# Kernel tuning notes

Measured on AMD Instinct MI355X. Metric: run time of the kernel, lower is better.

Reference implementation:

```python
import jax, jax.numpy as jnp
import numpy as np

N, BS, DIM, SIZE = 512, 64, 256, 8192

def setup_inputs() -> dict:
    key = jax.random.key(0)
    k1, k2 = jax.random.split(key)
    seq = jax.random.normal(k1, (N, BS, DIM), dtype=jnp.float32)
    # codebook initialized Uniform[-1, 1] as in _reset_parameters
    vocab = jax.random.uniform(k2, (SIZE, DIM), dtype=jnp.float32, minval=-1.0, maxval=1.0)
    return {"seq": seq, "vocab": vocab}

def reference(seq, vocab):
    n, bs, d = seq.shape
    x = seq.reshape(n * bs, d)                                   # [T, D]
    # squared euclidean distances; argmin identical to cdist(p=2).argmin
    x2 = jnp.sum(x * x, axis=-1, keepdims=True)                  # [T, 1]
    v2 = jnp.sum(vocab * vocab, axis=-1)                         # [K]
    d2 = x2 - 2.0 * (x @ vocab.T) + v2                           # [T, K]
    ingredients = jnp.argmin(d2, axis=1)                          # [T]
    out = jnp.take(vocab, ingredients, axis=0).reshape(n, bs, d)  # quantized seq
    return out, ingredients.reshape(n, bs)
```

## Files before the change

### kernel.cpp

```cpp
#include <hip/hip_runtime.h>

#define T_TOTAL 32768
#define D       256
#define K       8192
#define BQ      64
#define KSPLIT  4
#define KSLICE  (K / KSPLIT)
#define NSLICE  (KSPLIT * 4)
#define NCT32   (K / 32)
#define KT_STRIDE (NCT32 * 64 * 8)
#define NQB     (T_TOTAL / BQ)

typedef _Float16 half4f   __attribute__((ext_vector_type(4)));
typedef _Float16 half8f   __attribute__((ext_vector_type(8)));
typedef float    floatx16 __attribute__((ext_vector_type(16)));

#define PARTIAL_F 1048576
#define BHALVES   2097152

__device__ __forceinline__ _Float16 hi16(float x) { return (_Float16)x; }
__device__ __forceinline__ _Float16 lo16(float x, _Float16 h) { return (_Float16)(x - (float)h); }
__device__ __forceinline__ void split4(float4 v, half4f& h, half4f& l) {
    _Float16 hx = hi16(v.x), hy = hi16(v.y), hz = hi16(v.z), hw = hi16(v.w);
    h = (half4f){hx, hy, hz, hw};
    l = (half4f){lo16(v.x, hx), lo16(v.y, hy), lo16(v.z, hz), lo16(v.w, hw)};
}

__global__ void prep_kernel(const float* __restrict__ vocab,
                            _Float16* __restrict__ bhi, _Float16* __restrict__ blo,
                            float* __restrict__ hv2) {
    const int ct = blockIdx.x;
    const int t  = threadIdx.x;
    const int k4 = t & 63;
    const int w  = t >> 6;
    const float4* voc4 = (const float4*)vocab;
    const int kt = k4 >> 2;
    const int q  = k4 & 3;
    const int fl = 32 * (q >> 1);
    const int i0 = (q & 1) * 4;
    float ss[8];
    #pragma unroll
    for (int ci = 0; ci < 8; ++ci) {
        int cc = w * 8 + ci;
        float4 v = voc4[(size_t)(ct * 32 + cc) * (D / 4) + k4];
        half4f hh, ll;
        split4(v, hh, ll);
        size_t off = (((size_t)kt * NCT32 + ct) * 64 + (cc + fl)) * 8 + i0;
        *(half4f*)&bhi[off] = hh;
        *(half4f*)&blo[off] = ll;
        ss[ci] = v.x * v.x + v.y * v.y + v.z * v.z + v.w * v.w;
    }
    #pragma unroll
    for (int ci = 0; ci < 8; ++ci) {
        float s = ss[ci];
        #pragma unroll
        for (int off = 32; off; off >>= 1) s += __shfl_down(s, off, 64);
        if ((t & 63) == 0) hv2[ct * 32 + w * 8 + ci] = 0.5f * s;
    }
}

__launch_bounds__(256, 2)
__global__ void argmin_kernel(const float* __restrict__ seq,
                              const _Float16* __restrict__ bhi,
                              const _Float16* __restrict__ blo,
                              const float* __restrict__ hv2,
                              float2* __restrict__ partial) {
    __shared__ _Float16 AhL[2 * 16 * 64 * 8];
    __shared__ _Float16 AlL[2 * 16 * 64 * 8];

    const int t    = threadIdx.x;
    const int lane = t & 63;
    const int wn   = t >> 6;
    const int bi   = blockIdx.x;
    const int slice = (bi & 7) >> 1;
    const int qb    = (bi >> 3) * 2 + (bi & 1);
    const int q0   = qb * BQ;
    const int k0   = slice * KSLICE;

    const float4* seq4 = (const float4*)seq;

    #pragma unroll
    for (int i = 0; i < 16; ++i) {
        int f   = t + 256 * i;
        int row = f >> 6;
        int d4  = f & 63;
        float4 v = seq4[(size_t)(q0 + row) * (D / 4) + d4];
        half4f h, l;
        split4(v, h, l);
        int kt = d4 >> 2, qq = d4 & 3;
        int off = (((((row >> 5) * 16 + kt) * 64) + ((row & 31) + 32 * (qq >> 1))) * 8
                   + (qq & 1) * 4)
                  ^ (kt << 3);
        *(half4f*)&AhL[off] = h;
        *(half4f*)&AlL[off] = l;
    }
    __syncthreads();

    float best[32];
    int   bidx[32];
    #pragma unroll
    for (int b = 0; b < 32; ++b) { best[b] = 3.4e38f; bidx[b] = 0; }

    const _Float16* bh_l = bhi + (size_t)lane * 8;
    const _Float16* bl_l = blo + (size_t)lane * 8;

    for (int c0i = 0; c0i < KSLICE / 256; ++c0i) {
        const int c0  = k0 + c0i * 256;
        const int ct0 = (c0 >> 5) + wn * 2;
        const size_t cb = (size_t)ct0 * 512;

        floatx16 acc[2][2];
        #pragma unroll
        for (int mi = 0; mi < 2; ++mi)
            #pragma unroll
            for (int nj = 0; nj < 2; ++nj)
                #pragma unroll
                for (int r = 0; r < 16; ++r) acc[mi][nj][r] = 0.0f;

        half8f bh0[2], bl0[2], bh1[2], bl1[2];
        half8f ah0[2], al0[2], ah1[2], al1[2];
        #pragma unroll
        for (int nj = 0; nj < 2; ++nj) {
            bh0[nj] = *(const half8f*)&bh_l[cb + nj * 512];
            bl0[nj] = *(const half8f*)&bl_l[cb + nj * 512];
        }
        #pragma unroll
        for (int mi = 0; mi < 2; ++mi) {
            const int ao = ((mi * 16) * 64 + lane) * 8;
            ah0[mi] = *(const half8f*)&AhL[ao];
            al0[mi] = *(const half8f*)&AlL[ao];
        }

        #pragma unroll 1
        for (int kt2 = 0; kt2 < 8; ++kt2) {
            const int kt = kt2 * 2;
            {
                const size_t kb = (size_t)(kt + 1) * KT_STRIDE + cb;
                #pragma unroll
                for (int nj = 0; nj < 2; ++nj) {
                    bh1[nj] = *(const half8f*)&bh_l[kb + nj * 512];
                    bl1[nj] = *(const half8f*)&bl_l[kb + nj * 512];
                }
                #pragma unroll
                for (int mi = 0; mi < 2; ++mi) {
                    const int ao = (((mi * 16 + kt + 1) * 64 + lane) * 8) ^ ((kt + 1) << 3);
                    ah1[mi] = *(const half8f*)&AhL[ao];
                    al1[mi] = *(const half8f*)&AlL[ao];
                }
            }
            #pragma unroll
            for (int nj = 0; nj < 2; ++nj)
                #pragma unroll
                for (int mi = 0; mi < 2; ++mi)
                    acc[mi][nj] = __builtin_amdgcn_mfma_f32_32x32x16_f16(al0[mi], bh0[nj], acc[mi][nj], 0, 0, 0);
            #pragma unroll
            for (int nj = 0; nj < 2; ++nj)
                #pragma unroll
                for (int mi = 0; mi < 2; ++mi)
                    acc[mi][nj] = __builtin_amdgcn_mfma_f32_32x32x16_f16(ah0[mi], bl0[nj], acc[mi][nj], 0, 0, 0);
            #pragma unroll
            for (int nj = 0; nj < 2; ++nj)
                #pragma unroll
                for (int mi = 0; mi < 2; ++mi)
                    acc[mi][nj] = __builtin_amdgcn_mfma_f32_32x32x16_f16(ah0[mi], bh0[nj], acc[mi][nj], 0, 0, 0);
            if (kt2 < 7) {
                const size_t kb = (size_t)(kt + 2) * KT_STRIDE + cb;
                #pragma unroll
                for (int nj = 0; nj < 2; ++nj) {
                    bh0[nj] = *(const half8f*)&bh_l[kb + nj * 512];
                    bl0[nj] = *(const half8f*)&bl_l[kb + nj * 512];
                }
                #pragma unroll
                for (int mi = 0; mi < 2; ++mi) {
                    const int ao = (((mi * 16 + kt + 2) * 64 + lane) * 8) ^ ((kt + 2) << 3);
                    ah0[mi] = *(const half8f*)&AhL[ao];
                    al0[mi] = *(const half8f*)&AlL[ao];
                }
            }
            #pragma unroll
            for (int nj = 0; nj < 2; ++nj)
                #pragma unroll
                for (int mi = 0; mi < 2; ++mi)
                    acc[mi][nj] = __builtin_amdgcn_mfma_f32_32x32x16_f16(al1[mi], bh1[nj], acc[mi][nj], 0, 0, 0);
            #pragma unroll
            for (int nj = 0; nj < 2; ++nj)
                #pragma unroll
                for (int mi = 0; mi < 2; ++mi)
                    acc[mi][nj] = __builtin_amdgcn_mfma_f32_32x32x16_f16(ah1[mi], bl1[nj], acc[mi][nj], 0, 0, 0);
            #pragma unroll
            for (int nj = 0; nj < 2; ++nj)
                #pragma unroll
                for (int mi = 0; mi < 2; ++mi)
                    acc[mi][nj] = __builtin_amdgcn_mfma_f32_32x32x16_f16(ah1[mi], bh1[nj], acc[mi][nj], 0, 0, 0);
        }

        #pragma unroll
        for (int nj = 0; nj < 2; ++nj) {
            int c = c0 + (wn * 2 + nj) * 32 + (lane & 31);
            float hv = hv2[c];
            #pragma unroll
            for (int mi = 0; mi < 2; ++mi)
                #pragma unroll
                for (int r = 0; r < 16; ++r) {
                    float s = hv - acc[mi][nj][r];
                    int b = mi * 16 + r;
                    if (s < best[b]) { best[b] = s; bidx[b] = c; }
                }
        }
    }

    #pragma unroll
    for (int off = 1; off < 32; off <<= 1) {
        #pragma unroll
        for (int b = 0; b < 32; ++b) {
            float ob = __shfl_xor(best[b], off, 64);
            int   oi = __shfl_xor(bidx[b], off, 64);
            if (ob < best[b] || (ob == best[b] && oi < bidx[b])) {
                best[b] = ob; bidx[b] = oi;
            }
        }
    }
    if ((lane & 31) == 0) {
        const size_t sl = (size_t)(slice * 4 + wn) * T_TOTAL;
        const int rowadd = (lane >> 5) * 4;
        #pragma unroll
        for (int mi = 0; mi < 2; ++mi)
            #pragma unroll
            for (int r = 0; r < 16; ++r) {
                int qr = q0 + mi * 32 + (r & 3) + 8 * (r >> 2) + rowadd;
                partial[sl + qr] = make_float2(best[mi * 16 + r], (float)bidx[mi * 16 + r]);
            }
    }
}

__global__ void redgather_kernel(const float* __restrict__ vocab,
                                 const float2* __restrict__ partial,
                                 float* __restrict__ out) {
    int r    = blockIdx.x * 4 + (threadIdx.x >> 6);
    int lane = threadIdx.x & 63;
    float bm = 3.4e38f;
    int   bi = 0x7fffffff;
    if (lane < 16) {
        float2 p = partial[(size_t)lane * T_TOTAL + r];
        bm = p.x; bi = (int)p.y;
    }
    #pragma unroll
    for (int off = 1; off < 16; off <<= 1) {
        float ob = __shfl_xor(bm, off, 64);
        int   oi = __shfl_xor(bi, off, 64);
        if (ob < bm || (ob == bm && oi < bi)) { bm = ob; bi = oi; }
    }
    int k = __shfl(bi, 0, 64);
    const float4* src = (const float4*)(vocab + (size_t)k * D);
    float4*       dst = (float4*)(out + (size_t)r * D);
    dst[lane] = src[lane];
    if (lane == 0) out[(size_t)T_TOTAL * D + r] = (float)k;
}

__global__ void reduce_kernel(const float2* __restrict__ partial, int* __restrict__ idx) {
    int q = blockIdx.x * 256 + threadIdx.x;
    float bm = 3.4e38f;
    int   bi = 0x7fffffff;
    #pragma unroll
    for (int s = 0; s < NSLICE; ++s) {
        float2 p = partial[(size_t)s * T_TOTAL + q];
        int pi = (int)p.y;
        if (p.x < bm || (p.x == bm && pi < bi)) { bm = p.x; bi = pi; }
    }
    idx[q] = bi;
}

__global__ void gather_kernel(const float* __restrict__ vocab,
                              const int* __restrict__ idx,
                              float* __restrict__ out) {
    int r    = blockIdx.x * 4 + (threadIdx.x >> 6);
    int lane = threadIdx.x & 63;
    int k = idx[r];
    const float4* src = (const float4*)(vocab + (size_t)k * D);
    float4*       dst = (float4*)(out + (size_t)r * D);
    dst[lane] = src[lane];
    if (lane == 0) out[(size_t)T_TOTAL * D + r] = (float)k;
}

extern "C" void kernel_launch(void* const* d_in, const int* in_sizes, int n_in,
                              void* d_out, int out_size, void* d_ws, size_t ws_size,
                              hipStream_t stream) {
    const float* seq   = (const float*)d_in[0];
    const float* vocab = (const float*)d_in[1];
    float* out = (float*)d_out;

    float* hv2 = (float*)d_ws;
    _Float16* bhi = (_Float16*)(out + PARTIAL_F);
    _Float16* blo = bhi + BHALVES;

    const size_t need_ws = (size_t)(K + 2 * NSLICE * T_TOTAL) * sizeof(float) + 256;
    const bool fused = ws_size >= need_ws;

    hipLaunchKernelGGL(prep_kernel, dim3(NCT32), dim3(256), 0, stream, vocab, bhi, blo, hv2);

    if (fused) {
        float2* partial = (float2*)(hv2 + K);
        hipLaunchKernelGGL(argmin_kernel,    dim3(NQB * KSPLIT), dim3(256), 0, stream,
                           seq, bhi, blo, hv2, partial);
        hipLaunchKernelGGL(redgather_kernel, dim3(T_TOTAL / 4),  dim3(256), 0, stream,
                           vocab, partial, out);
    } else {
        float2* partial = (float2*)d_out;
        int* idx = (int*)(hv2 + K);
        hipLaunchKernelGGL(argmin_kernel, dim3(NQB * KSPLIT), dim3(256), 0, stream,
                           seq, bhi, blo, hv2, partial);
        hipLaunchKernelGGL(reduce_kernel, dim3(T_TOTAL / 256), dim3(256), 0, stream, partial, idx);
        hipLaunchKernelGGL(gather_kernel, dim3(T_TOTAL / 4),   dim3(256), 0, stream, vocab, idx, out);
    }
}
```

Measured before the change: 480.4 us.

## Deepen register prefetch pipeline across codebook tiles and pack argmin indices

Restructures the MFMA main loop into a 4-stage register pipeline where B fragments are prefetched two k-steps ahead and the prefetch continues across 256-column chunks, so the next chunk's loads overlap the current chunk's epilogue. MFMA bursts are wrapped in s_setprio to favour the matrix issue, and hv2 loads are hoisted to the top of each chunk. The per-row argmin indices are packed two per 32-bit register (16-bit each) to cut VGPR pressure from the extra prefetch buffers. The deeper pipeline raises register use, which may lower occupancy or cause spills. The packing relies on indices fitting in 16 bits, which holds for K=8192.

```diff
diff --git a/kernel.cpp b/kernel.cpp
--- a/kernel.cpp
+++ b/kernel.cpp
@@ -96,18 +96,65 @@
     }
     __syncthreads();
 
-    float best[32];
-    int   bidx[32];
-    #pragma unroll
-    for (int b = 0; b < 32; ++b) { best[b] = 3.4e38f; bidx[b] = 0; }
+    float    best[32];
+    unsigned bidxp[16];
+    #pragma unroll
+    for (int b = 0; b < 32; ++b) best[b] = 3.4e38f;
+    #pragma unroll
+    for (int b = 0; b < 16; ++b) bidxp[b] = 0u;
 
     const _Float16* bh_l = bhi + (size_t)lane * 8;
     const _Float16* bl_l = blo + (size_t)lane * 8;
 
+#define PF_B(BH, BL, X) do {                                                   \
+        const size_t kb_ = (size_t)((X) & 15) * KT_STRIDE + cb                 \
+                           + (size_t)((X) >> 4) * 4096;                        \
+        BH[0] = *(const half8f*)&bh_l[kb_];                                    \
+        BH[1] = *(const half8f*)&bh_l[kb_ + 512];                              \
+        BL[0] = *(const half8f*)&bl_l[kb_];                                    \
+        BL[1] = *(const half8f*)&bl_l[kb_ + 512];                              \
+    } while (0)
+
+#define PF_A(AH, AL, X) do {                                                   \
+        const int x_ = (X) & 15;                                               \
+        const int a0_ = (((x_) * 64 + lane) * 8) ^ (x_ << 3);                  \
+        const int a1_ = (((16 + x_) * 64 + lane) * 8) ^ (x_ << 3);             \
+        AH[0] = *(const half8f*)&AhL[a0_];  AL[0] = *(const half8f*)&AlL[a0_]; \
+        AH[1] = *(const half8f*)&AhL[a1_];  AL[1] = *(const half8f*)&AlL[a1_]; \
+    } while (0)
+
+#define MFMA_BURST(AH, AL, BH, BL) do {                                                          \
+        __builtin_amdgcn_s_setprio(1);                                                           \
+        acc[0][0] = __builtin_amdgcn_mfma_f32_32x32x16_f16(AL[0], BH[0], acc[0][0], 0, 0, 0);    \
+        acc[1][0] = __builtin_amdgcn_mfma_f32_32x32x16_f16(AL[1], BH[0], acc[1][0], 0, 0, 0);    \
+        acc[0][1] = __builtin_amdgcn_mfma_f32_32x32x16_f16(AL[0], BH[1], acc[0][1], 0, 0, 0);    \
+        acc[1][1] = __builtin_amdgcn_mfma_f32_32x32x16_f16(AL[1], BH[1], acc[1][1], 0, 0, 0);    \
+        acc[0][0] = __builtin_amdgcn_mfma_f32_32x32x16_f16(AH[0], BL[0], acc[0][0], 0, 0, 0);    \
+        acc[1][0] = __builtin_amdgcn_mfma_f32_32x32x16_f16(AH[1], BL[0], acc[1][0], 0, 0, 0);    \
+        acc[0][1] = __builtin_amdgcn_mfma_f32_32x32x16_f16(AH[0], BL[1], acc[0][1], 0, 0, 0);    \
+        acc[1][1] = __builtin_amdgcn_mfma_f32_32x32x16_f16(AH[1], BL[1], acc[1][1], 0, 0, 0);    \
+        acc[0][0] = __builtin_amdgcn_mfma_f32_32x32x16_f16(AH[0], BH[0], acc[0][0], 0, 0, 0);    \
+        acc[1][0] = __builtin_amdgcn_mfma_f32_32x32x16_f16(AH[1], BH[0], acc[1][0], 0, 0, 0);    \
+        acc[0][1] = __builtin_amdgcn_mfma_f32_32x32x16_f16(AH[0], BH[1], acc[0][1], 0, 0, 0);    \
+        acc[1][1] = __builtin_amdgcn_mfma_f32_32x32x16_f16(AH[1], BH[1], acc[1][1], 0, 0, 0);    \
+        __builtin_amdgcn_s_setprio(0);                                                           \
+    } while (0)
+
+    half8f bh0[2], bl0[2], bh1[2], bl1[2], bh2[2], bl2[2], bh3[2], bl3[2];
+    half8f ah0[2], al0[2], ah1[2], al1[2];
+
+    size_t cb = ((size_t)(k0 >> 5) + wn * 2) * 512;
+
+    PF_B(bh0, bl0, 0);
+    PF_B(bh1, bl1, 1);
+    PF_A(ah0, al0, 0);
+
+    #pragma unroll 1
     for (int c0i = 0; c0i < KSLICE / 256; ++c0i) {
-        const int c0  = k0 + c0i * 256;
-        const int ct0 = (c0 >> 5) + wn * 2;
-        const size_t cb = (size_t)ct0 * 512;
+        const int c0 = k0 + c0i * 256;
+
+        const float hvv0 = hv2[c0 + (wn * 2 + 0) * 32 + (lane & 31)];
+        const float hvv1 = hv2[c0 + (wn * 2 + 1) * 32 + (lane & 31)];
 
         floatx16 acc[2][2];
         #pragma unroll
@@ -117,97 +164,45 @@
                 #pragma unroll
                 for (int r = 0; r < 16; ++r) acc[mi][nj][r] = 0.0f;
 
-        half8f bh0[2], bl0[2], bh1[2], bl1[2];
-        half8f ah0[2], al0[2], ah1[2], al1[2];
+        #pragma unroll 1
+        for (int g = 0; g < 4; ++g) {
+            const int kt = g * 4;
+            PF_B(bh2, bl2, kt + 2);  PF_A(ah1, al1, kt + 1);
+            MFMA_BURST(ah0, al0, bh0, bl0);
+            PF_B(bh3, bl3, kt + 3);  PF_A(ah0, al0, kt + 2);
+            MFMA_BURST(ah1, al1, bh1, bl1);
+            PF_B(bh0, bl0, kt + 4);  PF_A(ah1, al1, kt + 3);
+            MFMA_BURST(ah0, al0, bh2, bl2);
+            PF_B(bh1, bl1, kt + 5);  PF_A(ah0, al0, kt + 4);
+            MFMA_BURST(ah1, al1, bh3, bl3);
+        }
+        cb += 4096;
+
         #pragma unroll
         for (int nj = 0; nj < 2; ++nj) {
-            bh0[nj] = *(const half8f*)&bh_l[cb + nj * 512];
-            bl0[nj] = *(const half8f*)&bl_l[cb + nj * 512];
-        }
-        #pragma unroll
-        for (int mi = 0; mi < 2; ++mi) {
-            const int ao = ((mi * 16) * 64 + lane) * 8;
-            ah0[mi] = *(const half8f*)&AhL[ao];
-            al0[mi] = *(const half8f*)&AlL[ao];
-        }
-
-        #pragma unroll 1
-        for (int kt2 = 0; kt2 < 8; ++kt2) {
-            const int kt = kt2 * 2;
-            {
-                const size_t kb = (size_t)(kt + 1) * KT_STRIDE + cb;
-                #pragma unroll
-                for (int nj = 0; nj < 2; ++nj) {
-                    bh1[nj] = *(const half8f*)&bh_l[kb + nj * 512];
-                    bl1[nj] = *(const half8f*)&bl_l[kb + nj * 512];
-                }
-                #pragma unroll
-                for (int mi = 0; mi < 2; ++mi) {
-                    const int ao = (((mi * 16 + kt + 1) * 64 + lane) * 8) ^ ((kt + 1) << 3);
-                    ah1[mi] = *(const half8f*)&AhL[ao];
-                    al1[mi] = *(const half8f*)&AlL[ao];
-                }
-            }
-            #pragma unroll
-            for (int nj = 0; nj < 2; ++nj)
-                #pragma unroll
-                for (int mi = 0; mi < 2; ++mi)
-                    acc[mi][nj] = __builtin_amdgcn_mfma_f32_32x32x16_f16(al0[mi], bh0[nj], acc[mi][nj], 0, 0, 0);
-            #pragma unroll
-            for (int nj = 0; nj < 2; ++nj)
-                #pragma unroll
-                for (int mi = 0; mi < 2; ++mi)
-                    acc[mi][nj] = __builtin_amdgcn_mfma_f32_32x32x16_f16(ah0[mi], bl0[nj], acc[mi][nj], 0, 0, 0);
-            #pragma unroll
-            for (int nj = 0; nj < 2; ++nj)
-                #pragma unroll
-                for (int mi = 0; mi < 2; ++mi)
-                    acc[mi][nj] = __builtin_amdgcn_mfma_f32_32x32x16_f16(ah0[mi], bh0[nj], acc[mi][nj], 0, 0, 0);
-            if (kt2 < 7) {
-                const size_t kb = (size_t)(kt + 2) * KT_STRIDE + cb;
-                #pragma unroll
-                for (int nj = 0; nj < 2; ++nj) {
-                    bh0[nj] = *(const half8f*)&bh_l[kb + nj * 512];
-                    bl0[nj] = *(const half8f*)&bl_l[kb + nj * 512];
-                }
-                #pragma unroll
-                for (int mi = 0; mi < 2; ++mi) {
-                    const int ao = (((mi * 16 + kt + 2) * 64 + lane) * 8) ^ ((kt + 2) << 3);
-                    ah0[mi] = *(const half8f*)&AhL[ao];
-                    al0[mi] = *(const half8f*)&AlL[ao];
-                }
-            }
-            #pragma unroll
-            for (int nj = 0; nj < 2; ++nj)
-                #pragma unroll
-                for (int mi = 0; mi < 2; ++mi)
-                    acc[mi][nj] = __builtin_amdgcn_mfma_f32_32x32x16_f16(al1[mi], bh1[nj], acc[mi][nj], 0, 0, 0);
-            #pragma unroll
-            for (int nj = 0; nj < 2; ++nj)
-                #pragma unroll
-                for (int mi = 0; mi < 2; ++mi)
-                    acc[mi][nj] = __builtin_amdgcn_mfma_f32_32x32x16_f16(ah1[mi], bl1[nj], acc[mi][nj], 0, 0, 0);
-            #pragma unroll
-            for (int nj = 0; nj < 2; ++nj)
-                #pragma unroll
-                for (int mi = 0; mi < 2; ++mi)
-                    acc[mi][nj] = __builtin_amdgcn_mfma_f32_32x32x16_f16(ah1[mi], bh1[nj], acc[mi][nj], 0, 0, 0);
-        }
-
-        #pragma unroll
-        for (int nj = 0; nj < 2; ++nj) {
-            int c = c0 + (wn * 2 + nj) * 32 + (lane & 31);
-            float hv = hv2[c];
+            const float hv = nj ? hvv1 : hvv0;
+            const int c = c0 + (wn * 2 + nj) * 32 + (lane & 31);
+            const unsigned clo = (unsigned)c;
+            const unsigned chi = (unsigned)c << 16;
             #pragma unroll
             for (int mi = 0; mi < 2; ++mi)
                 #pragma unroll
-                for (int r = 0; r < 16; ++r) {
-                    float s = hv - acc[mi][nj][r];
-                    int b = mi * 16 + r;
-                    if (s < best[b]) { best[b] = s; bidx[b] = c; }
+                for (int r = 0; r < 16; r += 2) {
+                    const int b = mi * 16 + r;
+                    float s0 = hv - acc[mi][nj][r];
+                    float s1 = hv - acc[mi][nj][r + 1];
+                    unsigned w = bidxp[b >> 1];
+                    if (s0 < best[b])     { best[b] = s0;     w = (w & 0xFFFF0000u) | clo; }
+                    if (s1 < best[b + 1]) { best[b + 1] = s1; w = (w & 0x0000FFFFu) | chi; }
+                    bidxp[b >> 1] = w;
                 }
         }
     }
+
+    int bidx[32];
+    #pragma unroll
+    for (int b = 0; b < 32; ++b)
+        bidx[b] = (b & 1) ? (int)(bidxp[b >> 1] >> 16) : (int)(bidxp[b >> 1] & 0xFFFFu);
 
     #pragma unroll
     for (int off = 1; off < 32; off <<= 1) {
@@ -231,6 +226,9 @@
                 partial[sl + qr] = make_float2(best[mi * 16 + r], (float)bidx[mi * 16 + r]);
             }
     }
+#undef PF_B
+#undef PF_A
+#undef MFMA_BURST
 }
 
 __global__ void redgather_kernel(const float* __restrict__ vocab,
```

New measurement: 494.3 us. 2.9% more time.
